# Kernel tuning notes

Hardware: AMD Instinct MI355X
Metric: run time of the kernel (lower is better)

## Reference

```python
import jax, jax.numpy as jnp
import numpy as np

N = 100000   # nodes
E = 1600000  # edges
F = 128      # feature dim == Dense units
R = 50       # relations
BN_EPS = 1e-3  # keras BatchNormalization default epsilon


def setup_inputs() -> dict:
    key = jax.random.key(0)
    ks = jax.random.split(key, 8)
    x = jax.random.normal(ks[0], (N, F), dtype=jnp.float32)
    edge_rows = jax.random.randint(ks[1], (E,), 0, N, dtype=jnp.int32)
    edge_cols = jax.random.randint(ks[2], (E,), 0, N, dtype=jnp.int32)
    edge_vals = jax.random.uniform(ks[3], (E,), dtype=jnp.float32)
    rel_ids = jax.random.randint(ks[4], (E,), 0, R, dtype=jnp.int32)
    relation_coeffs = jax.random.uniform(ks[5], (R,), dtype=jnp.float32)
    coeff_kernel = jax.random.normal(ks[6], (N, 1), dtype=jnp.float32) * 0.05
    dense_kernel = jax.random.normal(ks[7], (F, F), dtype=jnp.float32) / np.sqrt(F).astype(np.float32)
    dense_bias = jnp.zeros((F,), dtype=jnp.float32)
    bn_gamma = jnp.ones((F,), dtype=jnp.float32)
    bn_beta = jnp.zeros((F,), dtype=jnp.float32)
    bn_mean = jnp.zeros((F,), dtype=jnp.float32)
    bn_var = jnp.ones((F,), dtype=jnp.float32)
    return {
        "x": x, "edge_rows": edge_rows, "edge_cols": edge_cols,
        "edge_vals": edge_vals, "rel_ids": rel_ids,
        "relation_coeffs": relation_coeffs, "coeff_kernel": coeff_kernel,
        "dense_kernel": dense_kernel, "dense_bias": dense_bias,
        "bn_gamma": bn_gamma, "bn_beta": bn_beta,
        "bn_mean": bn_mean, "bn_var": bn_var,
    }


def reference(x, edge_rows, edge_cols, edge_vals, rel_ids,
              relation_coeffs, coeff_kernel, dense_kernel, dense_bias,
              bn_gamma, bn_beta, bn_mean, bn_var):
    # BatchNorm (inference: moving statistics)
    h = (x - bn_mean) * jax.lax.rsqrt(bn_var + BN_EPS) * bn_gamma + bn_beta  # [N, F]
    # relation_coeff_adj2: edge weight = A.values * (rel_coeffs[rel] + 1)^-1
    w = edge_vals / (relation_coeffs[rel_ids] + 1.0)  # [E]
    # SpMM: out[i] = sum_{(i,j) in edges} w_e * h[j]
    msgs = w[:, None] * h[edge_cols]                   # [E, F]
    agg = jax.ops.segment_sum(msgs, edge_rows, num_segments=N)  # [N, F]
    # CoeffLayer(mul=True): inputs * (kernel + 1)
    pre = agg + h * (coeff_kernel + 1.0)               # [N, F]
    # Dense
    return pre @ dense_kernel + dense_bias             # [N, F]
```

## Files before the change

kernel.cpp:

```cpp
#include <hip/hip_runtime.h>
#include <stdint.h>

#define N_NODES 100000
#define N_EDGES 1600000
#define FDIM 128
#define NREL 50
#define BN_EPS 1e-3f
#define N_PAD 100096
#define NBUCK 1563
#define EPB 8192
#define NBLK 196
#define HBLK 6250
#define SCAP 1536
#define SORTN 1792

typedef short short8_t __attribute__((ext_vector_type(8)));
typedef float f32x4_t __attribute__((ext_vector_type(4)));

__device__ __forceinline__ uint32_t f2bf(float f) {
    union { float f; uint32_t u; } v; v.f = f;
    uint32_t u = v.u;
    return (u + 0x7FFFu + ((u >> 16) & 1u)) >> 16;
}
__device__ __forceinline__ float bflo(uint32_t p) {
    union { uint32_t u; float f; } v; v.u = p << 16; return v.f;
}
__device__ __forceinline__ float bfhi(uint32_t p) {
    union { uint32_t u; float f; } v; v.u = p & 0xFFFF0000u; return v.f;
}

__global__ __launch_bounds__(512) void pre_kernel(
        const float* __restrict__ x, const int* __restrict__ rows,
        const int* __restrict__ cols, const float* __restrict__ vals,
        const int* __restrict__ rels, const float* __restrict__ relc,
        const float* __restrict__ gamma, const float* __restrict__ beta,
        const float* __restrict__ mean, const float* __restrict__ var,
        const float* __restrict__ W,
        uint2* __restrict__ h, uint16_t* __restrict__ WT,
        int* __restrict__ gcur, uint2* __restrict__ staging) {
    __shared__ int lh[NBUCK];
    __shared__ float lrel[NREL];
    int b = blockIdx.x, t = threadIdx.x;
    if (b < NBLK) {
        if (t < NREL) lrel[t] = 1.0f / (relc[t] + 1.0f);
        for (int i = t; i < NBUCK; i += 512) lh[i] = 0;
        __syncthreads();
        int e0 = b * EPB, e1 = min(e0 + EPB, N_EDGES);
        for (int e = e0 + t; e < e1; e += 512)
            atomicAdd(&lh[rows[e] >> 6], 1);
        __syncthreads();
        for (int i = t; i < NBUCK; i += 512) {
            int c = lh[i];
            int base = c ? atomicAdd(&gcur[i], c) : 0;
            lh[i] = i * SCAP + base;
        }
        __syncthreads();
        for (int e = e0 + t; e < e1; e += 512) {
            int r = rows[e];
            int bk = r >> 6;
            float w = vals[e] * lrel[rels[e]];
            int p = atomicAdd(&lh[bk], 1);
            if (p < (bk + 1) * SCAP) {
                uint2 s;
                s.x = (uint32_t)cols[e] | ((uint32_t)(r & 63) << 20);
                s.y = __float_as_uint(w);
                staging[p] = s;
            }
        }
    } else if (b == NBLK) {
        for (int idx = t; idx < FDIM * FDIM; idx += 512) {
            int f = idx >> 7, k = idx & 127;
            WT[idx] = (uint16_t)f2bf(W[k * FDIM + f]);
        }
    } else {
        int i4 = (b - NBLK - 1) * 512 + t;
        int cg = (i4 & 31) * 4;
        float4 xv = ((const float4*)x)[i4];
        float4 g4 = *(const float4*)(gamma + cg);
        float4 b4 = *(const float4*)(beta + cg);
        float4 m4 = *(const float4*)(mean + cg);
        float4 v4 = *(const float4*)(var + cg);
        float s0 = g4.x * rsqrtf(v4.x + BN_EPS);
        float s1 = g4.y * rsqrtf(v4.y + BN_EPS);
        float s2 = g4.z * rsqrtf(v4.z + BN_EPS);
        float s3 = g4.w * rsqrtf(v4.w + BN_EPS);
        uint2 o;
        o.x = f2bf((xv.x - m4.x) * s0 + b4.x) | (f2bf((xv.y - m4.y) * s1 + b4.y) << 16);
        o.y = f2bf((xv.z - m4.z) * s2 + b4.z) | (f2bf((xv.w - m4.w) * s3 + b4.w) << 16);
        h[i4] = o;
    }
}

__global__ __launch_bounds__(512, 8) void sg_kernel(
        const uint32_t* __restrict__ h, const int* __restrict__ gcur,
        const uint2* __restrict__ staging, const float* __restrict__ ck,
        const uint16_t* __restrict__ WT, const float* __restrict__ bias,
        float* __restrict__ out) {
    __shared__ uint32_t lp[64 * 64];
    __shared__ uint2 sorted[SORTN];
    __shared__ int lh[64];
    __shared__ int lcur[64];
    __shared__ uint2 rinfo[64];
    uint2* led = (uint2*)lp;

    int t = threadIdx.x;
    int wv = t >> 6, lane = t & 63;
    int b = blockIdx.x, r0 = b << 6;

    if (t < 64) lh[t] = 0;
    __syncthreads();
    int cnt = min(gcur[b], SCAP);
    const uint2* sge = staging + (size_t)b * SCAP;
    for (int e = t; e < cnt; e += 512) {
        uint2 s = sge[e];
        led[e] = s;
        atomicAdd(&lh[(s.x >> 20) & 63], 1);
    }
    __syncthreads();
    if (t < 64) {
        int v = lh[t];
        int pv = (v + 3) & ~3;
        int s = pv;
        for (int d = 1; d < 64; d <<= 1) {
            int u = __shfl_up(s, d);
            if (t >= d) s += u;
        }
        int start = s - pv;
        lcur[t] = start;
        uint2 ri; ri.x = (uint32_t)start; ri.y = (uint32_t)(start + pv);
        rinfo[t] = ri;
        uint2 z; z.x = 0; z.y = 0;
        for (int k = v; k < pv; ++k) sorted[start + k] = z;
    }
    __syncthreads();
    for (int e = t; e < cnt; e += 512) {
        uint2 s = led[e];
        int rl = (s.x >> 20) & 63;
        int p = atomicAdd(&lcur[rl], 1);
        uint2 o; o.x = s.x & 0xFFFFFu; o.y = s.y;
        sorted[p] = o;
    }
    __syncthreads();

#pragma unroll
    for (int i = 0; i < 4; ++i) {
        int rlA = wv * 8 + 2 * i, rlB = rlA + 1;
        int rA = r0 + rlA, rB = r0 + rlB;
        uint2 ia = rinfo[rlA], ib = rinfo[rlB];
        int eA  = __builtin_amdgcn_readfirstlane((int)ia.x);
        int e1A = __builtin_amdgcn_readfirstlane((int)ia.y);
        int eB  = __builtin_amdgcn_readfirstlane((int)ib.x);
        int e1B = __builtin_amdgcn_readfirstlane((int)ib.y);
        float axA = 0.f, ayA = 0.f, axB = 0.f, ayB = 0.f;
        if (rA < N_NODES) {
            uint32_t p = h[(uint32_t)rA * 64u + lane];
            float c = ck[rA] + 1.0f;
            axA = c * bflo(p); ayA = c * bfhi(p);
        }
        if (rB < N_NODES) {
            uint32_t p = h[(uint32_t)rB * 64u + lane];
            float c = ck[rB] + 1.0f;
            axB = c * bflo(p); ayB = c * bfhi(p);
        }
        while (eA < e1A && eB < e1B) {
            uint4 a0 = *(const uint4*)&sorted[eA];
            uint4 a1 = *(const uint4*)&sorted[eA + 2];
            uint4 b0 = *(const uint4*)&sorted[eB];
            uint4 b1 = *(const uint4*)&sorted[eB + 2];
            uint32_t qa0 = h[a0.x * 64u + lane];
            uint32_t qa1 = h[a0.z * 64u + lane];
            uint32_t qa2 = h[a1.x * 64u + lane];
            uint32_t qa3 = h[a1.z * 64u + lane];
            uint32_t qb0 = h[b0.x * 64u + lane];
            uint32_t qb1 = h[b0.z * 64u + lane];
            uint32_t qb2 = h[b1.x * 64u + lane];
            uint32_t qb3 = h[b1.z * 64u + lane];
            float wa0 = __uint_as_float(a0.y), wa1 = __uint_as_float(a0.w);
            float wa2 = __uint_as_float(a1.y), wa3 = __uint_as_float(a1.w);
            float wb0 = __uint_as_float(b0.y), wb1 = __uint_as_float(b0.w);
            float wb2 = __uint_as_float(b1.y), wb3 = __uint_as_float(b1.w);
            axA += wa0 * bflo(qa0); ayA += wa0 * bfhi(qa0);
            axA += wa1 * bflo(qa1); ayA += wa1 * bfhi(qa1);
            axA += wa2 * bflo(qa2); ayA += wa2 * bfhi(qa2);
            axA += wa3 * bflo(qa3); ayA += wa3 * bfhi(qa3);
            axB += wb0 * bflo(qb0); ayB += wb0 * bfhi(qb0);
            axB += wb1 * bflo(qb1); ayB += wb1 * bfhi(qb1);
            axB += wb2 * bflo(qb2); ayB += wb2 * bfhi(qb2);
            axB += wb3 * bflo(qb3); ayB += wb3 * bfhi(qb3);
            eA += 4; eB += 4;
        }
        while (eA < e1A) {
            uint4 a0 = *(const uint4*)&sorted[eA];
            uint4 a1 = *(const uint4*)&sorted[eA + 2];
            uint32_t qa0 = h[a0.x * 64u + lane];
            uint32_t qa1 = h[a0.z * 64u + lane];
            uint32_t qa2 = h[a1.x * 64u + lane];
            uint32_t qa3 = h[a1.z * 64u + lane];
            float wa0 = __uint_as_float(a0.y), wa1 = __uint_as_float(a0.w);
            float wa2 = __uint_as_float(a1.y), wa3 = __uint_as_float(a1.w);
            axA += wa0 * bflo(qa0); ayA += wa0 * bfhi(qa0);
            axA += wa1 * bflo(qa1); ayA += wa1 * bfhi(qa1);
            axA += wa2 * bflo(qa2); ayA += wa2 * bfhi(qa2);
            axA += wa3 * bflo(qa3); ayA += wa3 * bfhi(qa3);
            eA += 4;
        }
        while (eB < e1B) {
            uint4 b0 = *(const uint4*)&sorted[eB];
            uint4 b1 = *(const uint4*)&sorted[eB + 2];
            uint32_t qb0 = h[b0.x * 64u + lane];
            uint32_t qb1 = h[b0.z * 64u + lane];
            uint32_t qb2 = h[b1.x * 64u + lane];
            uint32_t qb3 = h[b1.z * 64u + lane];
            float wb0 = __uint_as_float(b0.y), wb1 = __uint_as_float(b0.w);
            float wb2 = __uint_as_float(b1.y), wb3 = __uint_as_float(b1.w);
            axB += wb0 * bflo(qb0); ayB += wb0 * bfhi(qb0);
            axB += wb1 * bflo(qb1); ayB += wb1 * bfhi(qb1);
            axB += wb2 * bflo(qb2); ayB += wb2 * bfhi(qb2);
            axB += wb3 * bflo(qb3); ayB += wb3 * bfhi(qb3);
            eB += 4;
        }
        lp[rlA * 64 + (lane ^ ((rlA & 7) << 2))] = f2bf(axA) | (f2bf(ayA) << 16);
        lp[rlB * 64 + (lane ^ ((rlB & 7) << 2))] = f2bf(axB) | (f2bf(ayB) << 16);
    }
    __syncthreads();

    int m = lane & 15, q = lane >> 4;
    int rl0 = (wv & 3) << 4;
    int colb = (wv >> 2) << 6;
    int rlm = rl0 + m;
    short8_t a[4];
#pragma unroll
    for (int tt = 0; tt < 4; ++tt) {
        int w0 = (q * 4 + tt * 16) ^ ((rlm & 7) << 2);
        a[tt] = *(const short8_t*)&lp[rlm * 64 + w0];
    }
#pragma unroll
    for (int ct = 0; ct < 4; ++ct) {
        int col0 = colb + ct * 16;
        const uint16_t* brow = WT + (size_t)(col0 + m) * FDIM + q * 8;
        f32x4_t acc = {0.f, 0.f, 0.f, 0.f};
#pragma unroll
        for (int tt = 0; tt < 4; ++tt) {
            short8_t bb = *(const short8_t*)(brow + tt * 32);
            acc = __builtin_amdgcn_mfma_f32_16x16x32_bf16(a[tt], bb, acc, 0, 0, 0);
        }
        float bs = bias[col0 + m];
#pragma unroll
        for (int r = 0; r < 4; ++r) {
            int row = r0 + rl0 + q * 4 + r;
            if (row < N_NODES)
                out[(size_t)row * FDIM + col0 + m] = acc[r] + bs;
        }
    }
}

extern "C" void kernel_launch(void* const* d_in, const int* in_sizes, int n_in,
                              void* d_out, int out_size, void* d_ws, size_t ws_size,
                              hipStream_t stream) {
    const float* x     = (const float*)d_in[0];
    const int*   erows = (const int*)d_in[1];
    const int*   ecols = (const int*)d_in[2];
    const float* evals = (const float*)d_in[3];
    const int*   erels = (const int*)d_in[4];
    const float* relc  = (const float*)d_in[5];
    const float* ck    = (const float*)d_in[6];
    const float* W     = (const float*)d_in[7];
    const float* bias  = (const float*)d_in[8];
    const float* gamma = (const float*)d_in[9];
    const float* beta  = (const float*)d_in[10];
    const float* mean  = (const float*)d_in[11];
    const float* var   = (const float*)d_in[12];
    float* out = (float*)d_out;

    char* wp = (char*)d_ws;
    auto alloc = [&](size_t bytes) {
        char* p = wp;
        wp += (bytes + 255) & ~(size_t)255;
        return (void*)p;
    };
    uint16_t* h      = (uint16_t*)alloc((size_t)N_PAD * FDIM * 2);
    uint2* staging   = (uint2*)alloc((size_t)NBUCK * SCAP * 8);
    int* gcur        = (int*)alloc((size_t)NBUCK * 4);
    uint16_t* WT     = (uint16_t*)alloc(FDIM * FDIM * 2);
    if ((size_t)(wp - (char*)d_ws) > ws_size) return;

    hipMemsetAsync(gcur, 0, (size_t)NBUCK * 4, stream);
    pre_kernel<<<NBLK + 1 + HBLK, 512, 0, stream>>>(
        x, erows, ecols, evals, erels, relc, gamma, beta, mean, var, W,
        (uint2*)h, WT, gcur, staging);
    sg_kernel<<<NBUCK, 512, 0, stream>>>((const uint32_t*)h, gcur, staging, ck,
                                         WT, bias, out);
}
```

Baseline: 256.9 us.

## Locally sort edges by bucket in shared memory before scattering to staging

The edge-binning blocks now prefix-scan their per-bucket counts and build a shared-memory permutation that groups each block's edges by destination bucket. Consecutive threads then write consecutive staging slots, so the global scatter becomes more contiguous instead of random 8-byte writes. The cost is an extra pass with shared atomics, a serial 64-lane scan over 1563 buckets, more shared memory, and gathered re-reads of rows, cols, vals and rels through the permutation.

Result: no change. 259.0 us (+0.8%).

```diff
diff --git a/kernel.cpp b/kernel.cpp
--- a/kernel.cpp
+++ b/kernel.cpp
@@ -39,6 +39,9 @@
         uint2* __restrict__ h, uint16_t* __restrict__ WT,
         int* __restrict__ gcur, uint2* __restrict__ staging) {
     __shared__ int lh[NBUCK];
+    __shared__ int cur[NBUCK];
+    __shared__ int comb[NBUCK];
+    __shared__ uint16_t perm16[EPB];
     __shared__ float lrel[NREL];
     int b = blockIdx.x, t = threadIdx.x;
     if (b < NBLK) {
@@ -46,25 +49,51 @@
         for (int i = t; i < NBUCK; i += 512) lh[i] = 0;
         __syncthreads();
         int e0 = b * EPB, e1 = min(e0 + EPB, N_EDGES);
+        int cntb = e1 - e0;
         for (int e = e0 + t; e < e1; e += 512)
             atomicAdd(&lh[rows[e] >> 6], 1);
         __syncthreads();
+        if (t < 64) {
+            int carry = 0;
+            for (int seg = 0; seg < (NBUCK + 63) / 64; ++seg) {
+                int idx = seg * 64 + t;
+                int v = (idx < NBUCK) ? lh[idx] : 0;
+                int s = v;
+                for (int d = 1; d < 64; d <<= 1) {
+                    int u = __shfl_up(s, d);
+                    if (t >= d) s += u;
+                }
+                if (idx < NBUCK) lh[idx] = carry + s - v;
+                carry += __shfl(s, 63);
+            }
+        }
+        __syncthreads();
         for (int i = t; i < NBUCK; i += 512) {
-            int c = lh[i];
-            int base = c ? atomicAdd(&gcur[i], c) : 0;
-            lh[i] = i * SCAP + base;
+            int bs = lh[i];
+            int bn = (i + 1 < NBUCK) ? lh[i + 1] : cntb;
+            int c = bn - bs;
+            cur[i] = bs;
+            int gb = i * SCAP + (c ? atomicAdd(&gcur[i], c) : 0);
+            comb[i] = gb - bs;
         }
         __syncthreads();
         for (int e = e0 + t; e < e1; e += 512) {
+            int bk = rows[e] >> 6;
+            int pos = atomicAdd(&cur[bk], 1);
+            perm16[pos] = (uint16_t)(e - e0);
+        }
+        __syncthreads();
+        for (int p = t; p < cntb; p += 512) {
+            int e = e0 + perm16[p];
             int r = rows[e];
             int bk = r >> 6;
             float w = vals[e] * lrel[rels[e]];
-            int p = atomicAdd(&lh[bk], 1);
-            if (p < (bk + 1) * SCAP) {
+            int dest = comb[bk] + p;
+            if (dest < (bk + 1) * SCAP) {
                 uint2 s;
                 s.x = (uint32_t)cols[e] | ((uint32_t)(r & 63) << 20);
                 s.y = __float_as_uint(w);
-                staging[p] = s;
+                staging[dest] = s;
             }
         }
     } else if (b == NBLK) {
```

## Split each wave into two half-waves gathering alternate edges with 8-byte loads

Applied to the files above, without the earlier changes.

Each 64-lane wave now runs as two 32-lane halves. Each lane loads 8 bytes (4 bf16 features) of a neighbour row, and the two halves handle interleaved edges, with the partial sums combined through a cross-half shuffle at the end. Edge segments are padded to multiples of 8 instead of 4, and the sorted LDS buffer grows to hold the extra padding. The aim is to double the number of rows gathered in flight per instruction and use wider loads, at the cost of more padding edges, a larger LDS footprint and the final shuffle reduction.

After: 255.1 us. About the same (-0.7%).

```diff
diff --git a/kernel.cpp b/kernel.cpp
--- a/kernel.cpp
+++ b/kernel.cpp
@@ -12,7 +12,7 @@
 #define NBLK 196
 #define HBLK 6250
 #define SCAP 1536
-#define SORTN 1792
+#define SORTN 1984
 
 typedef short short8_t __attribute__((ext_vector_type(8)));
 typedef float f32x4_t __attribute__((ext_vector_type(4)));
@@ -91,8 +91,13 @@
     }
 }
 
+#define GSTEP(d, q, s0, s1, s2, s3) {                 \
+    float w_ = __uint_as_float((d).y);                \
+    s0 += w_ * bflo((q).x); s1 += w_ * bfhi((q).x);   \
+    s2 += w_ * bflo((q).y); s3 += w_ * bfhi((q).y); }
+
 __global__ __launch_bounds__(512, 8) void sg_kernel(
-        const uint32_t* __restrict__ h, const int* __restrict__ gcur,
+        const uint32_t* __restrict__ hw, const int* __restrict__ gcur,
         const uint2* __restrict__ staging, const float* __restrict__ ck,
         const uint16_t* __restrict__ WT, const float* __restrict__ bias,
         float* __restrict__ out) {
@@ -102,9 +107,11 @@
     __shared__ int lcur[64];
     __shared__ uint2 rinfo[64];
     uint2* led = (uint2*)lp;
+    const uint2* h2 = (const uint2*)hw;
 
     int t = threadIdx.x;
     int wv = t >> 6, lane = t & 63;
+    int hl = lane & 31, hsel = lane >> 5;
     int b = blockIdx.x, r0 = b << 6;
 
     if (t < 64) lh[t] = 0;
@@ -119,7 +126,7 @@
     __syncthreads();
     if (t < 64) {
         int v = lh[t];
-        int pv = (v + 3) & ~3;
+        int pv = (v + 7) & ~7;
         int s = pv;
         for (int d = 1; d < 64; d <<= 1) {
             int u = __shfl_up(s, d);
@@ -151,76 +158,79 @@
         int e1A = __builtin_amdgcn_readfirstlane((int)ia.y);
         int eB  = __builtin_amdgcn_readfirstlane((int)ib.x);
         int e1B = __builtin_amdgcn_readfirstlane((int)ib.y);
-        float axA = 0.f, ayA = 0.f, axB = 0.f, ayB = 0.f;
-        if (rA < N_NODES) {
-            uint32_t p = h[(uint32_t)rA * 64u + lane];
-            float c = ck[rA] + 1.0f;
-            axA = c * bflo(p); ayA = c * bfhi(p);
-        }
-        if (rB < N_NODES) {
-            uint32_t p = h[(uint32_t)rB * 64u + lane];
-            float c = ck[rB] + 1.0f;
-            axB = c * bflo(p); ayB = c * bfhi(p);
-        }
+        int rsel = hsel ? rB : rA;
+        int rc = min(rsel, N_NODES - 1);
+        uint2 p = h2[(uint32_t)rc * 32u + hl];
+        float cv = ck[rc] + 1.0f;
+        cv = (rsel < N_NODES) ? cv : 0.0f;
+        float f0 = cv * bflo(p.x), f1 = cv * bfhi(p.x);
+        float f2 = cv * bflo(p.y), f3 = cv * bfhi(p.y);
+        float a0 = hsel ? 0.f : f0, a1 = hsel ? 0.f : f1;
+        float a2 = hsel ? 0.f : f2, a3 = hsel ? 0.f : f3;
+        float b0 = hsel ? f0 : 0.f, b1 = hsel ? f1 : 0.f;
+        float b2 = hsel ? f2 : 0.f, b3 = hsel ? f3 : 0.f;
+
         while (eA < e1A && eB < e1B) {
-            uint4 a0 = *(const uint4*)&sorted[eA];
-            uint4 a1 = *(const uint4*)&sorted[eA + 2];
-            uint4 b0 = *(const uint4*)&sorted[eB];
-            uint4 b1 = *(const uint4*)&sorted[eB + 2];
-            uint32_t qa0 = h[a0.x * 64u + lane];
-            uint32_t qa1 = h[a0.z * 64u + lane];
-            uint32_t qa2 = h[a1.x * 64u + lane];
-            uint32_t qa3 = h[a1.z * 64u + lane];
-            uint32_t qb0 = h[b0.x * 64u + lane];
-            uint32_t qb1 = h[b0.z * 64u + lane];
-            uint32_t qb2 = h[b1.x * 64u + lane];
-            uint32_t qb3 = h[b1.z * 64u + lane];
-            float wa0 = __uint_as_float(a0.y), wa1 = __uint_as_float(a0.w);
-            float wa2 = __uint_as_float(a1.y), wa3 = __uint_as_float(a1.w);
-            float wb0 = __uint_as_float(b0.y), wb1 = __uint_as_float(b0.w);
-            float wb2 = __uint_as_float(b1.y), wb3 = __uint_as_float(b1.w);
-            axA += wa0 * bflo(qa0); ayA += wa0 * bfhi(qa0);
-            axA += wa1 * bflo(qa1); ayA += wa1 * bfhi(qa1);
-            axA += wa2 * bflo(qa2); ayA += wa2 * bfhi(qa2);
-            axA += wa3 * bflo(qa3); ayA += wa3 * bfhi(qa3);
-            axB += wb0 * bflo(qb0); ayB += wb0 * bfhi(qb0);
-            axB += wb1 * bflo(qb1); ayB += wb1 * bfhi(qb1);
-            axB += wb2 * bflo(qb2); ayB += wb2 * bfhi(qb2);
-            axB += wb3 * bflo(qb3); ayB += wb3 * bfhi(qb3);
-            eA += 4; eB += 4;
+            uint2 dA0 = sorted[eA + 0 + hsel];
+            uint2 dA1 = sorted[eA + 2 + hsel];
+            uint2 dA2 = sorted[eA + 4 + hsel];
+            uint2 dA3 = sorted[eA + 6 + hsel];
+            uint2 dB0 = sorted[eB + 0 + hsel];
+            uint2 dB1 = sorted[eB + 2 + hsel];
+            uint2 dB2 = sorted[eB + 4 + hsel];
+            uint2 dB3 = sorted[eB + 6 + hsel];
+            uint2 qA0 = h2[dA0.x * 32u + hl];
+            uint2 qA1 = h2[dA1.x * 32u + hl];
+            uint2 qA2 = h2[dA2.x * 32u + hl];
+            uint2 qA3 = h2[dA3.x * 32u + hl];
+            uint2 qB0 = h2[dB0.x * 32u + hl];
+            uint2 qB1 = h2[dB1.x * 32u + hl];
+            uint2 qB2 = h2[dB2.x * 32u + hl];
+            uint2 qB3 = h2[dB3.x * 32u + hl];
+            GSTEP(dA0, qA0, a0, a1, a2, a3); GSTEP(dA1, qA1, a0, a1, a2, a3);
+            GSTEP(dA2, qA2, a0, a1, a2, a3); GSTEP(dA3, qA3, a0, a1, a2, a3);
+            GSTEP(dB0, qB0, b0, b1, b2, b3); GSTEP(dB1, qB1, b0, b1, b2, b3);
+            GSTEP(dB2, qB2, b0, b1, b2, b3); GSTEP(dB3, qB3, b0, b1, b2, b3);
+            eA += 8; eB += 8;
         }
         while (eA < e1A) {
-            uint4 a0 = *(const uint4*)&sorted[eA];
-            uint4 a1 = *(const uint4*)&sorted[eA + 2];
-            uint32_t qa0 = h[a0.x * 64u + lane];
-            uint32_t qa1 = h[a0.z * 64u + lane];
-            uint32_t qa2 = h[a1.x * 64u + lane];
-            uint32_t qa3 = h[a1.z * 64u + lane];
-            float wa0 = __uint_as_float(a0.y), wa1 = __uint_as_float(a0.w);
-            float wa2 = __uint_as_float(a1.y), wa3 = __uint_as_float(a1.w);
-            axA += wa0 * bflo(qa0); ayA += wa0 * bfhi(qa0);
-            axA += wa1 * bflo(qa1); ayA += wa1 * bfhi(qa1);
-            axA += wa2 * bflo(qa2); ayA += wa2 * bfhi(qa2);
-            axA += wa3 * bflo(qa3); ayA += wa3 * bfhi(qa3);
-            eA += 4;
+            uint2 dA0 = sorted[eA + 0 + hsel];
+            uint2 dA1 = sorted[eA + 2 + hsel];
+            uint2 dA2 = sorted[eA + 4 + hsel];
+            uint2 dA3 = sorted[eA + 6 + hsel];
+            uint2 qA0 = h2[dA0.x * 32u + hl];
+            uint2 qA1 = h2[dA1.x * 32u + hl];
+            uint2 qA2 = h2[dA2.x * 32u + hl];
+            uint2 qA3 = h2[dA3.x * 32u + hl];
+            GSTEP(dA0, qA0, a0, a1, a2, a3); GSTEP(dA1, qA1, a0, a1, a2, a3);
+            GSTEP(dA2, qA2, a0, a1, a2, a3); GSTEP(dA3, qA3, a0, a1, a2, a3);
+            eA += 8;
         }
         while (eB < e1B) {
-            uint4 b0 = *(const uint4*)&sorted[eB];
-            uint4 b1 = *(const uint4*)&sorted[eB + 2];
-            uint32_t qb0 = h[b0.x * 64u + lane];
-            uint32_t qb1 = h[b0.z * 64u + lane];
-            uint32_t qb2 = h[b1.x * 64u + lane];
-            uint32_t qb3 = h[b1.z * 64u + lane];
-            float wb0 = __uint_as_float(b0.y), wb1 = __uint_as_float(b0.w);
-            float wb2 = __uint_as_float(b1.y), wb3 = __uint_as_float(b1.w);
-            axB += wb0 * bflo(qb0); ayB += wb0 * bfhi(qb0);
-            axB += wb1 * bflo(qb1); ayB += wb1 * bfhi(qb1);
-            axB += wb2 * bflo(qb2); ayB += wb2 * bfhi(qb2);
-            axB += wb3 * bflo(qb3); ayB += wb3 * bfhi(qb3);
-            eB += 4;
-        }
-        lp[rlA * 64 + (lane ^ ((rlA & 7) << 2))] = f2bf(axA) | (f2bf(ayA) << 16);
-        lp[rlB * 64 + (lane ^ ((rlB & 7) << 2))] = f2bf(axB) | (f2bf(ayB) << 16);
+            uint2 dB0 = sorted[eB + 0 + hsel];
+            uint2 dB1 = sorted[eB + 2 + hsel];
+            uint2 dB2 = sorted[eB + 4 + hsel];
+            uint2 dB3 = sorted[eB + 6 + hsel];
+            uint2 qB0 = h2[dB0.x * 32u + hl];
+            uint2 qB1 = h2[dB1.x * 32u + hl];
+            uint2 qB2 = h2[dB2.x * 32u + hl];
+            uint2 qB3 = h2[dB3.x * 32u + hl];
+            GSTEP(dB0, qB0, b0, b1, b2, b3); GSTEP(dB1, qB1, b0, b1, b2, b3);
+            GSTEP(dB2, qB2, b0, b1, b2, b3); GSTEP(dB3, qB3, b0, b1, b2, b3);
+            eB += 8;
+        }
+        a0 += __shfl_xor(a0, 32, 64); a1 += __shfl_xor(a1, 32, 64);
+        a2 += __shfl_xor(a2, 32, 64); a3 += __shfl_xor(a3, 32, 64);
+        b0 += __shfl_xor(b0, 32, 64); b1 += __shfl_xor(b1, 32, 64);
+        b2 += __shfl_xor(b2, 32, 64); b3 += __shfl_xor(b3, 32, 64);
+        if (lane < 32) {
+            int cA = (rlA & 7) << 2, cB = (rlB & 7) << 2;
+            uint2 wA, wB;
+            wA.x = f2bf(a0) | (f2bf(a1) << 16); wA.y = f2bf(a2) | (f2bf(a3) << 16);
+            wB.x = f2bf(b0) | (f2bf(b1) << 16); wB.y = f2bf(b2) | (f2bf(b3) << 16);
+            *(uint2*)&lp[rlA * 64 + ((2 * hl) ^ cA)] = wA;
+            *(uint2*)&lp[rlB * 64 + ((2 * hl) ^ cB)] = wB;
+        }
     }
     __syncthreads();
 
```
